# Optimization experiments

Measured on AMD Instinct MI355X. Metric: run time of the kernel, lower is better.

The kernel has to match this reference:

```python
import jax, jax.numpy as jnp
import numpy as np

N = 500_000
B = 8192
D = 128
EPS = 1e-5


def setup_inputs() -> dict:
    key = jax.random.key(0)
    ks = jax.random.split(key, 8)
    h = jax.random.normal(ks[0], (N, D), dtype=jnp.float32)
    batch = jnp.sort(jax.random.randint(ks[1], (N,), 0, B)).astype(jnp.int64)
    vn_h = jax.random.normal(ks[2], (B, D), dtype=jnp.float32)
    # layer 0 MLP params: Linear(D,D) -> LayerNorm(D) -> ReLU -> Linear(D,D)
    W1 = jax.random.normal(ks[3], (D, D), dtype=jnp.float32) * 0.02
    b1 = jnp.zeros((D,), dtype=jnp.float32)
    ln_g = jnp.ones((D,), dtype=jnp.float32)
    ln_b = jnp.zeros((D,), dtype=jnp.float32)
    W2 = jax.random.normal(ks[4], (D, D), dtype=jnp.float32) * 0.02
    b2 = jnp.zeros((D,), dtype=jnp.float32)
    return {"h": h, "batch": batch, "vn_h": vn_h, "W1": W1, "b1": b1,
            "ln_g": ln_g, "ln_b": ln_b, "W2": W2, "b2": b2}


def _layernorm(x, g, b):
    mu = jnp.mean(x, axis=-1, keepdims=True)
    var = jnp.mean(jnp.square(x - mu), axis=-1, keepdims=True)
    return (x - mu) * jax.lax.rsqrt(var + EPS) * g + b


def reference(h, batch, vn_h, W1, b1, ln_g, ln_b, W2, b2):
    batch = batch.astype(jnp.int32)
    # global_mean_pool: segment mean of node features per graph  [B, D]
    seg_sum = jax.ops.segment_sum(h, batch, num_segments=B)
    counts = jax.ops.segment_sum(jnp.ones((h.shape[0],), h.dtype), batch, num_segments=B)
    pooled = seg_sum / jnp.maximum(counts, 1.0)[:, None]
    vn_h_new = pooled + vn_h
    # vn MLP: Linear -> LayerNorm -> ReLU -> Linear
    x = vn_h_new @ W1.T + b1
    x = jax.nn.relu(_layernorm(x, ln_g, ln_b))
    vn_out = x @ W2.T + b2                      # [B, D]
    h_out = h + vn_out[batch]                   # broadcast gather back to nodes
    return h_out, vn_out
```

## Files before the change

### kernel.cpp

```cpp
#include <hip/hip_runtime.h>

#define DIM 128
#define EPS 1e-5f

typedef short           bf16x8 __attribute__((ext_vector_type(8)));
typedef unsigned short  u16x4  __attribute__((ext_vector_type(4)));
typedef float           f32x4  __attribute__((ext_vector_type(4)));

__device__ __forceinline__ unsigned short f2b(float f) {
    unsigned int u = __builtin_bit_cast(unsigned int, f);
    unsigned int r = (u + 0x7FFFu + ((u >> 16) & 1u)) >> 16;
    return (unsigned short)r;
}
__device__ __forceinline__ bf16x8 ldw8(const float* __restrict__ p) {
    f32x4 a = *reinterpret_cast<const f32x4*>(p);
    f32x4 b = *reinterpret_cast<const f32x4*>(p + 4);
    bf16x8 r;
    #pragma unroll
    for (int j = 0; j < 4; ++j) {
        r[j]     = (short)f2b(a[j]);
        r[j + 4] = (short)f2b(b[j]);
    }
    return r;
}

__global__ __launch_bounds__(256) void k_bounds(
    const int* __restrict__ batch, int* __restrict__ bounds, int n_nodes, int nb)
{
    const int idx = blockIdx.x * blockDim.x + threadIdx.x;
    if (idx > n_nodes) return;
    const int cur  = (idx < n_nodes) ? batch[idx] : nb;
    const int prev = (idx > 0) ? batch[idx - 1] : -1;
    for (int b = prev + 1; b <= cur; ++b) bounds[b] = idx;
}

__global__ __launch_bounds__(256) void k_pool(
    const float* __restrict__ h, const int* __restrict__ bounds,
    const float* __restrict__ vn, unsigned short* __restrict__ x_ws, int nb)
{
    const int wid  = (blockIdx.x * blockDim.x + threadIdx.x) >> 6;
    const int lane = threadIdx.x & 63;
    if (wid >= nb) return;
    const int rsub = lane >> 5;
    const int l32  = lane & 31;
    const int s = bounds[wid], e = bounds[wid + 1];

    const f32x4 z4 = (f32x4){0.f, 0.f, 0.f, 0.f};
    f32x4 a0 = z4, a1 = z4, a2 = z4, a3 = z4;
    int n = s;
    for (; n + 7 < e; n += 8) {
        const float* p = h + (size_t)(n + rsub) * DIM + l32 * 4;
        f32x4 x0 = *reinterpret_cast<const f32x4*>(p);
        f32x4 x1 = *reinterpret_cast<const f32x4*>(p + 2 * DIM);
        f32x4 x2 = *reinterpret_cast<const f32x4*>(p + 4 * DIM);
        f32x4 x3 = *reinterpret_cast<const f32x4*>(p + 6 * DIM);
        a0 += x0; a1 += x1; a2 += x2; a3 += x3;
    }
    for (; n + rsub < e; n += 2)
        a0 += *reinterpret_cast<const f32x4*>(h + (size_t)(n + rsub) * DIM + l32 * 4);
    a0 += a1; a2 += a3; a0 += a2;
    #pragma unroll
    for (int c = 0; c < 4; ++c) a0[c] += __shfl_xor(a0[c], 32);

    if (rsub == 0) {
        const int cnt = e - s;
        const float inv = 1.0f / (float)(cnt > 1 ? cnt : 1);
        f32x4 vv = *reinterpret_cast<const f32x4*>(vn + (size_t)wid * DIM + l32 * 4);
        u16x4 ov;
        #pragma unroll
        for (int q = 0; q < 4; ++q) ov[q] = f2b(fmaf(a0[q], inv, vv[q]));
        *reinterpret_cast<u16x4*>(x_ws + (size_t)wid * DIM + l32 * 4) = ov;
    }
}

__global__ __launch_bounds__(256) void k_mlp(
    const unsigned short* __restrict__ x_ws,
    const float* __restrict__ W1, const float* __restrict__ b1,
    const float* __restrict__ lng, const float* __restrict__ lnb,
    const float* __restrict__ W2, const float* __restrict__ b2v,
    float* __restrict__ vn_out)
{
    __shared__ unsigned short zt[4][16][136];

    const int wave  = threadIdx.x >> 6;
    const int lane  = threadIdx.x & 63;
    const int gtile = blockIdx.x * 4 + wave;
    const int row16 = lane & 15;
    const int kgrp  = lane >> 4;

    bf16x8 afrag[4];
    {
        const unsigned short* xp =
            x_ws + (size_t)(gtile * 16 + row16) * DIM + kgrp * 8;
        #pragma unroll
        for (int kk = 0; kk < 4; ++kk)
            afrag[kk] = *reinterpret_cast<const bf16x8*>(xp + kk * 32);
    }
    f32x4 acc[8];
    #pragma unroll
    for (int t = 0; t < 8; ++t) acc[t] = (f32x4){0.f, 0.f, 0.f, 0.f};
    #pragma unroll
    for (int t = 0; t < 8; ++t) {
        const float* wp = W1 + (size_t)(t * 16 + row16) * DIM + kgrp * 8;
        #pragma unroll
        for (int kk = 0; kk < 4; ++kk) {
            bf16x8 bfrag = ldw8(wp + kk * 32);
            acc[t] = __builtin_amdgcn_mfma_f32_16x16x32_bf16(afrag[kk], bfrag, acc[t], 0, 0, 0);
        }
    }

    float b1f[8], gf[8], bf_[8], b2f8[8];
    #pragma unroll
    for (int t = 0; t < 8; ++t) {
        const int f = t * 16 + row16;
        b1f[t]  = b1[f];
        gf[t]   = lng[f];
        bf_[t]  = lnb[f];
        b2f8[t] = b2v[f];
    }
    #pragma unroll
    for (int t = 0; t < 8; ++t)
        #pragma unroll
        for (int r = 0; r < 4; ++r) acc[t][r] += b1f[t];

    #pragma unroll
    for (int r = 0; r < 4; ++r) {
        float sm = 0.f, ss = 0.f;
        #pragma unroll
        for (int t = 0; t < 8; ++t) { sm += acc[t][r]; ss += acc[t][r] * acc[t][r]; }
        #pragma unroll
        for (int m = 1; m <= 8; m <<= 1) {
            sm += __shfl_xor(sm, m);
            ss += __shfl_xor(ss, m);
        }
        const float mu  = sm * (1.0f / 128.0f);
        const float var = ss * (1.0f / 128.0f) - mu * mu;
        const float rs  = rsqrtf(var + EPS);
        const int   gm  = kgrp * 4 + r;
        #pragma unroll
        for (int t = 0; t < 8; ++t) {
            float z = (acc[t][r] - mu) * rs * gf[t] + bf_[t];
            z = fmaxf(z, 0.f);
            zt[wave][gm][t * 16 + row16] = f2b(z);
        }
    }
    __syncthreads();

    bf16x8 afrag2[4];
    #pragma unroll
    for (int kk = 0; kk < 4; ++kk)
        afrag2[kk] = *reinterpret_cast<const bf16x8*>(&zt[wave][row16][kk * 32 + kgrp * 8]);

    f32x4 acc2[8];
    #pragma unroll
    for (int t = 0; t < 8; ++t) acc2[t] = (f32x4){0.f, 0.f, 0.f, 0.f};
    #pragma unroll
    for (int t = 0; t < 8; ++t) {
        const float* wp = W2 + (size_t)(t * 16 + row16) * DIM + kgrp * 8;
        #pragma unroll
        for (int kk = 0; kk < 4; ++kk) {
            bf16x8 bfrag = ldw8(wp + kk * 32);
            acc2[t] = __builtin_amdgcn_mfma_f32_16x16x32_bf16(afrag2[kk], bfrag, acc2[t], 0, 0, 0);
        }
    }

    #pragma unroll
    for (int r = 0; r < 4; ++r) {
        float* op = vn_out + (size_t)(gtile * 16 + kgrp * 4 + r) * DIM + row16;
        #pragma unroll
        for (int t = 0; t < 8; ++t)
            op[t * 16] = acc2[t][r] + b2f8[t];
    }
}

__global__ __launch_bounds__(256) void k_add(
    const float* __restrict__ h, const int* __restrict__ batch,
    const float* __restrict__ vn_out, float* __restrict__ h_out,
    int n_nodes)
{
    const long total = (long)n_nodes * 16;
    for (long u = (long)blockIdx.x * blockDim.x + threadIdx.x; u < total;
         u += (long)gridDim.x * blockDim.x) {
        const int n = (int)(u >> 4);
        const int c = ((int)u & 15) * 8;
        const float* hp = h + (size_t)n * DIM + c;
        f32x4 h0 = *reinterpret_cast<const f32x4*>(hp);
        f32x4 h1 = *reinterpret_cast<const f32x4*>(hp + 4);
        const int b = batch[n];
        const float* vp = vn_out + (size_t)b * DIM + c;
        f32x4 v0 = *reinterpret_cast<const f32x4*>(vp);
        f32x4 v1 = *reinterpret_cast<const f32x4*>(vp + 4);
        float* op = h_out + (size_t)n * DIM + c;
        __builtin_nontemporal_store(h0 + v0, reinterpret_cast<f32x4*>(op));
        __builtin_nontemporal_store(h1 + v1, reinterpret_cast<f32x4*>(op + 4));
    }
}

extern "C" void kernel_launch(void* const* d_in, const int* in_sizes, int n_in,
                              void* d_out, int out_size, void* d_ws, size_t ws_size,
                              hipStream_t stream)
{
    const float* h    = (const float*)d_in[0];
    const int*   bat  = (const int*)d_in[1];
    const float* vn   = (const float*)d_in[2];
    const float* W1   = (const float*)d_in[3];
    const float* b1   = (const float*)d_in[4];
    const float* lng  = (const float*)d_in[5];
    const float* lnb  = (const float*)d_in[6];
    const float* W2   = (const float*)d_in[7];
    const float* b2v  = (const float*)d_in[8];

    const int n_nodes = in_sizes[0] / DIM;
    const int nb      = in_sizes[2] / DIM;

    float* out    = (float*)d_out;
    float* h_out  = out;
    float* vn_out = out + (size_t)n_nodes * DIM;
    int*   bounds = (int*)d_ws;
    unsigned short* x_ws =
        (unsigned short*)((char*)d_ws + ((size_t)(nb + 1) * 4 + 255 & ~255ull));

    k_bounds<<<(n_nodes + 256) / 256, 256, 0, stream>>>(bat, bounds, n_nodes, nb);
    k_pool<<<nb / 4, 256, 0, stream>>>(h, bounds, vn, x_ws, nb);
    k_mlp<<<nb / 64, 256, 0, stream>>>(x_ws, W1, b1, lng, lnb, W2, b2v, vn_out);
    k_add<<<2048, 256, 0, stream>>>(h, bat, vn_out, h_out, n_nodes);
}
```

Before: 160.1 us.

## Fuse pooling, MLP and broadcast-add into one per-graph wave kernel

Replaces the separate pool, MLP and add kernels with a single kernel where each wave owns one graph. The wave sums that graph's nodes, runs both linear layers through MFMA with the pooled row padded into a 16-row tile via lane shuffles, then re-reads the graph's nodes to write h_out. Weights are converted to bf16 once in a small prep kernel instead of on every weight load. This removes the intermediate round trips and the per-node gather of batch indices. In exchange, 15 of the 16 MFMA rows do wasted work, and h is read twice within the same wave, which works best if the second read still hits cache. Writing vn_out and reading it back relies on a vmcnt wait and a volatile load within the wave.

```diff
diff --git a/kernel.cpp b/kernel.cpp
--- a/kernel.cpp
+++ b/kernel.cpp
@@ -3,25 +3,15 @@
 #define DIM 128
 #define EPS 1e-5f
 
-typedef short           bf16x8 __attribute__((ext_vector_type(8)));
-typedef unsigned short  u16x4  __attribute__((ext_vector_type(4)));
-typedef float           f32x4  __attribute__((ext_vector_type(4)));
+typedef short        bf16x8 __attribute__((ext_vector_type(8)));
+typedef unsigned int u32x4  __attribute__((ext_vector_type(4)));
+typedef float        f32x2  __attribute__((ext_vector_type(2)));
+typedef float        f32x4  __attribute__((ext_vector_type(4)));
 
 __device__ __forceinline__ unsigned short f2b(float f) {
     unsigned int u = __builtin_bit_cast(unsigned int, f);
     unsigned int r = (u + 0x7FFFu + ((u >> 16) & 1u)) >> 16;
     return (unsigned short)r;
-}
-__device__ __forceinline__ bf16x8 ldw8(const float* __restrict__ p) {
-    f32x4 a = *reinterpret_cast<const f32x4*>(p);
-    f32x4 b = *reinterpret_cast<const f32x4*>(p + 4);
-    bf16x8 r;
-    #pragma unroll
-    for (int j = 0; j < 4; ++j) {
-        r[j]     = (short)f2b(a[j]);
-        r[j + 4] = (short)f2b(b[j]);
-    }
-    return r;
 }
 
 __global__ __launch_bounds__(256) void k_bounds(
@@ -34,165 +24,172 @@
     for (int b = prev + 1; b <= cur; ++b) bounds[b] = idx;
 }
 
-__global__ __launch_bounds__(256) void k_pool(
+__global__ __launch_bounds__(256) void k_prep(
+    const float* __restrict__ W1, const float* __restrict__ W2,
+    unsigned short* __restrict__ Wb)
+{
+    const int i = blockIdx.x * blockDim.x + threadIdx.x;
+    if (i >= 32768) return;
+    const float v = (i < 16384) ? W1[i] : W2[i - 16384];
+    Wb[i] = f2b(v);
+}
+
+__global__ __launch_bounds__(256, 6) void k_fused(
     const float* __restrict__ h, const int* __restrict__ bounds,
-    const float* __restrict__ vn, unsigned short* __restrict__ x_ws, int nb)
+    const float* __restrict__ vn, const unsigned short* __restrict__ Wb,
+    const float* __restrict__ b1, const float* __restrict__ lng,
+    const float* __restrict__ lnb, const float* __restrict__ b2v,
+    float* __restrict__ vn_out, float* __restrict__ h_out)
 {
     const int wid  = (blockIdx.x * blockDim.x + threadIdx.x) >> 6;
     const int lane = threadIdx.x & 63;
-    if (wid >= nb) return;
-    const int rsub = lane >> 5;
-    const int l32  = lane & 31;
     const int s = bounds[wid], e = bounds[wid + 1];
 
-    const f32x4 z4 = (f32x4){0.f, 0.f, 0.f, 0.f};
-    f32x4 a0 = z4, a1 = z4, a2 = z4, a3 = z4;
+    const f32x2 z2 = (f32x2){0.f, 0.f};
+    f32x2 a0 = z2, a1 = z2, a2 = z2, a3 = z2, a4 = z2, a5 = z2, a6 = z2, a7 = z2;
     int n = s;
-    for (; n + 7 < e; n += 8) {
-        const float* p = h + (size_t)(n + rsub) * DIM + l32 * 4;
-        f32x4 x0 = *reinterpret_cast<const f32x4*>(p);
-        f32x4 x1 = *reinterpret_cast<const f32x4*>(p + 2 * DIM);
-        f32x4 x2 = *reinterpret_cast<const f32x4*>(p + 4 * DIM);
-        f32x4 x3 = *reinterpret_cast<const f32x4*>(p + 6 * DIM);
-        a0 += x0; a1 += x1; a2 += x2; a3 += x3;
-    }
-    for (; n + rsub < e; n += 2)
-        a0 += *reinterpret_cast<const f32x4*>(h + (size_t)(n + rsub) * DIM + l32 * 4);
-    a0 += a1; a2 += a3; a0 += a2;
-    #pragma unroll
-    for (int c = 0; c < 4; ++c) a0[c] += __shfl_xor(a0[c], 32);
-
-    if (rsub == 0) {
-        const int cnt = e - s;
-        const float inv = 1.0f / (float)(cnt > 1 ? cnt : 1);
-        f32x4 vv = *reinterpret_cast<const f32x4*>(vn + (size_t)wid * DIM + l32 * 4);
-        u16x4 ov;
-        #pragma unroll
-        for (int q = 0; q < 4; ++q) ov[q] = f2b(fmaf(a0[q], inv, vv[q]));
-        *reinterpret_cast<u16x4*>(x_ws + (size_t)wid * DIM + l32 * 4) = ov;
-    }
-}
-
-__global__ __launch_bounds__(256) void k_mlp(
-    const unsigned short* __restrict__ x_ws,
-    const float* __restrict__ W1, const float* __restrict__ b1,
-    const float* __restrict__ lng, const float* __restrict__ lnb,
-    const float* __restrict__ W2, const float* __restrict__ b2v,
-    float* __restrict__ vn_out)
-{
-    __shared__ unsigned short zt[4][16][136];
-
-    const int wave  = threadIdx.x >> 6;
-    const int lane  = threadIdx.x & 63;
-    const int gtile = blockIdx.x * 4 + wave;
+    for (; n + 8 <= e; n += 8) {
+        const float* p = h + (size_t)n * DIM + lane * 2;
+        a0 += *reinterpret_cast<const f32x2*>(p);
+        a1 += *reinterpret_cast<const f32x2*>(p + DIM);
+        a2 += *reinterpret_cast<const f32x2*>(p + 2 * DIM);
+        a3 += *reinterpret_cast<const f32x2*>(p + 3 * DIM);
+        a4 += *reinterpret_cast<const f32x2*>(p + 4 * DIM);
+        a5 += *reinterpret_cast<const f32x2*>(p + 5 * DIM);
+        a6 += *reinterpret_cast<const f32x2*>(p + 6 * DIM);
+        a7 += *reinterpret_cast<const f32x2*>(p + 7 * DIM);
+    }
+    for (; n < e; ++n)
+        a0 += *reinterpret_cast<const f32x2*>(h + (size_t)n * DIM + lane * 2);
+    a0 += a1; a2 += a3; a4 += a5; a6 += a7; a0 += a2; a4 += a6; a0 += a4;
+
+    const int cnt = e - s;
+    const float inv = 1.0f / (float)(cnt > 1 ? cnt : 1);
+    f32x2 vv = *reinterpret_cast<const f32x2*>(vn + (size_t)wid * DIM + lane * 2);
+    const unsigned int x01 =
+        (unsigned int)f2b(fmaf(a0[0], inv, vv[0])) |
+        ((unsigned int)f2b(fmaf(a0[1], inv, vv[1])) << 16);
+
     const int row16 = lane & 15;
     const int kgrp  = lane >> 4;
 
-    bf16x8 afrag[4];
-    {
-        const unsigned short* xp =
-            x_ws + (size_t)(gtile * 16 + row16) * DIM + kgrp * 8;
-        #pragma unroll
-        for (int kk = 0; kk < 4; ++kk)
-            afrag[kk] = *reinterpret_cast<const bf16x8*>(xp + kk * 32);
-    }
-    f32x4 acc[8];
-    #pragma unroll
-    for (int t = 0; t < 8; ++t) acc[t] = (f32x4){0.f, 0.f, 0.f, 0.f};
+    bf16x8 af[4];
+    #pragma unroll
+    for (int kt = 0; kt < 4; ++kt) {
+        const int sbase = kt * 16 + kgrp * 4;
+        u32x4 w;
+        w[0] = __shfl(x01, sbase + 0);
+        w[1] = __shfl(x01, sbase + 1);
+        w[2] = __shfl(x01, sbase + 2);
+        w[3] = __shfl(x01, sbase + 3);
+        af[kt] = __builtin_bit_cast(bf16x8, w);
+    }
+
+    f32x4 C[8];
+    #pragma unroll
+    for (int t = 0; t < 8; ++t) C[t] = (f32x4){0.f, 0.f, 0.f, 0.f};
     #pragma unroll
     for (int t = 0; t < 8; ++t) {
-        const float* wp = W1 + (size_t)(t * 16 + row16) * DIM + kgrp * 8;
-        #pragma unroll
-        for (int kk = 0; kk < 4; ++kk) {
-            bf16x8 bfrag = ldw8(wp + kk * 32);
-            acc[t] = __builtin_amdgcn_mfma_f32_16x16x32_bf16(afrag[kk], bfrag, acc[t], 0, 0, 0);
+        const unsigned short* wr = Wb + (size_t)(t * 16 + row16) * DIM + kgrp * 8;
+        #pragma unroll
+        for (int kt = 0; kt < 4; ++kt) {
+            bf16x8 bf = *reinterpret_cast<const bf16x8*>(wr + kt * 32);
+            C[t] = __builtin_amdgcn_mfma_f32_16x16x32_bf16(af[kt], bf, C[t], 0, 0, 0);
         }
     }
 
-    float b1f[8], gf[8], bf_[8], b2f8[8];
+    float y[8];
+    float gf[8], bf_[8], b2f8[8];
     #pragma unroll
     for (int t = 0; t < 8; ++t) {
         const int f = t * 16 + row16;
-        b1f[t]  = b1[f];
+        y[t]    = C[t][0] + b1[f];
         gf[t]   = lng[f];
         bf_[t]  = lnb[f];
         b2f8[t] = b2v[f];
     }
-    #pragma unroll
-    for (int t = 0; t < 8; ++t)
-        #pragma unroll
-        for (int r = 0; r < 4; ++r) acc[t][r] += b1f[t];
-
-    #pragma unroll
-    for (int r = 0; r < 4; ++r) {
-        float sm = 0.f, ss = 0.f;
-        #pragma unroll
-        for (int t = 0; t < 8; ++t) { sm += acc[t][r]; ss += acc[t][r] * acc[t][r]; }
-        #pragma unroll
-        for (int m = 1; m <= 8; m <<= 1) {
-            sm += __shfl_xor(sm, m);
-            ss += __shfl_xor(ss, m);
+
+    float sm = 0.f, ss = 0.f;
+    #pragma unroll
+    for (int t = 0; t < 8; ++t) { sm += y[t]; ss += y[t] * y[t]; }
+    #pragma unroll
+    for (int m = 1; m <= 8; m <<= 1) {
+        sm += __shfl_xor(sm, m);
+        ss += __shfl_xor(ss, m);
+    }
+    const float mu  = sm * (1.0f / 128.0f);
+    const float var = ss * (1.0f / 128.0f) - mu * mu;
+    const float rs  = rsqrtf(var + EPS);
+
+    unsigned int zp[4];
+    #pragma unroll
+    for (int kt = 0; kt < 4; ++kt) {
+        float zl = fmaxf((y[2 * kt]     - mu) * rs * gf[2 * kt]     + bf_[2 * kt],     0.f);
+        float zh = fmaxf((y[2 * kt + 1] - mu) * rs * gf[2 * kt + 1] + bf_[2 * kt + 1], 0.f);
+        zp[kt] = (unsigned int)f2b(zl) | ((unsigned int)f2b(zh) << 16);
+    }
+
+    const unsigned int hsel = kgrp >> 1;
+    const int sbase2 = (kgrp & 1) * 8;
+    bf16x8 zf[4];
+    #pragma unroll
+    for (int kt = 0; kt < 4; ++kt) {
+        u32x4 w;
+        #pragma unroll
+        for (int c2 = 0; c2 < 4; ++c2) {
+            unsigned int q0 = __shfl(zp[kt], sbase2 + 2 * c2);
+            unsigned int q1 = __shfl(zp[kt], sbase2 + 2 * c2 + 1);
+            unsigned int e0 = hsel ? (q0 >> 16) : (q0 & 0xFFFFu);
+            unsigned int e1 = hsel ? (q1 >> 16) : (q1 & 0xFFFFu);
+            w[c2] = e0 | (e1 << 16);
         }
-        const float mu  = sm * (1.0f / 128.0f);
-        const float var = ss * (1.0f / 128.0f) - mu * mu;
-        const float rs  = rsqrtf(var + EPS);
-        const int   gm  = kgrp * 4 + r;
-        #pragma unroll
-        for (int t = 0; t < 8; ++t) {
-            float z = (acc[t][r] - mu) * rs * gf[t] + bf_[t];
-            z = fmaxf(z, 0.f);
-            zt[wave][gm][t * 16 + row16] = f2b(z);
+        zf[kt] = __builtin_bit_cast(bf16x8, w);
+    }
+
+    f32x4 C2[8];
+    #pragma unroll
+    for (int t = 0; t < 8; ++t) C2[t] = (f32x4){0.f, 0.f, 0.f, 0.f};
+    #pragma unroll
+    for (int t = 0; t < 8; ++t) {
+        const unsigned short* wr =
+            Wb + 16384 + (size_t)(t * 16 + row16) * DIM + kgrp * 8;
+        #pragma unroll
+        for (int kt = 0; kt < 4; ++kt) {
+            bf16x8 bf = *reinterpret_cast<const bf16x8*>(wr + kt * 32);
+            C2[t] = __builtin_amdgcn_mfma_f32_16x16x32_bf16(zf[kt], bf, C2[t], 0, 0, 0);
         }
     }
-    __syncthreads();
-
-    bf16x8 afrag2[4];
-    #pragma unroll
-    for (int kk = 0; kk < 4; ++kk)
-        afrag2[kk] = *reinterpret_cast<const bf16x8*>(&zt[wave][row16][kk * 32 + kgrp * 8]);
-
-    f32x4 acc2[8];
-    #pragma unroll
-    for (int t = 0; t < 8; ++t) acc2[t] = (f32x4){0.f, 0.f, 0.f, 0.f};
-    #pragma unroll
-    for (int t = 0; t < 8; ++t) {
-        const float* wp = W2 + (size_t)(t * 16 + row16) * DIM + kgrp * 8;
-        #pragma unroll
-        for (int kk = 0; kk < 4; ++kk) {
-            bf16x8 bfrag = ldw8(wp + kk * 32);
-            acc2[t] = __builtin_amdgcn_mfma_f32_16x16x32_bf16(afrag2[kk], bfrag, acc2[t], 0, 0, 0);
-        }
-    }
-
-    #pragma unroll
-    for (int r = 0; r < 4; ++r) {
-        float* op = vn_out + (size_t)(gtile * 16 + kgrp * 4 + r) * DIM + row16;
+
+    if (lane < 16) {
         #pragma unroll
         for (int t = 0; t < 8; ++t)
-            op[t * 16] = acc2[t][r] + b2f8[t];
-    }
-}
-
-__global__ __launch_bounds__(256) void k_add(
-    const float* __restrict__ h, const int* __restrict__ batch,
-    const float* __restrict__ vn_out, float* __restrict__ h_out,
-    int n_nodes)
-{
-    const long total = (long)n_nodes * 16;
-    for (long u = (long)blockIdx.x * blockDim.x + threadIdx.x; u < total;
-         u += (long)gridDim.x * blockDim.x) {
-        const int n = (int)(u >> 4);
-        const int c = ((int)u & 15) * 8;
-        const float* hp = h + (size_t)n * DIM + c;
-        f32x4 h0 = *reinterpret_cast<const f32x4*>(hp);
-        f32x4 h1 = *reinterpret_cast<const f32x4*>(hp + 4);
-        const int b = batch[n];
-        const float* vp = vn_out + (size_t)b * DIM + c;
-        f32x4 v0 = *reinterpret_cast<const f32x4*>(vp);
-        f32x4 v1 = *reinterpret_cast<const f32x4*>(vp + 4);
-        float* op = h_out + (size_t)n * DIM + c;
-        __builtin_nontemporal_store(h0 + v0, reinterpret_cast<f32x4*>(op));
-        __builtin_nontemporal_store(h1 + v1, reinterpret_cast<f32x4*>(op + 4));
+            vn_out[(size_t)wid * DIM + t * 16 + row16] = C2[t][0] + b2f8[t];
+    }
+
+    asm volatile("s_waitcnt vmcnt(0)" ::: "memory");
+    volatile const float* vo = vn_out + (size_t)wid * DIM + lane * 2;
+    const float w0 = vo[0];
+    const float w1 = vo[1];
+    const f32x2 w = (f32x2){w0, w1};
+
+    n = s;
+    for (; n + 4 <= e; n += 4) {
+        const float* p = h + (size_t)n * DIM + lane * 2;
+        f32x2 r0 = *reinterpret_cast<const f32x2*>(p);
+        f32x2 r1 = *reinterpret_cast<const f32x2*>(p + DIM);
+        f32x2 r2 = *reinterpret_cast<const f32x2*>(p + 2 * DIM);
+        f32x2 r3 = *reinterpret_cast<const f32x2*>(p + 3 * DIM);
+        float* q = h_out + (size_t)n * DIM + lane * 2;
+        __builtin_nontemporal_store(r0 + w, reinterpret_cast<f32x2*>(q));
+        __builtin_nontemporal_store(r1 + w, reinterpret_cast<f32x2*>(q + DIM));
+        __builtin_nontemporal_store(r2 + w, reinterpret_cast<f32x2*>(q + 2 * DIM));
+        __builtin_nontemporal_store(r3 + w, reinterpret_cast<f32x2*>(q + 3 * DIM));
+    }
+    for (; n < e; ++n) {
+        const float* p = h + (size_t)n * DIM + lane * 2;
+        f32x2 r0 = *reinterpret_cast<const f32x2*>(p);
+        float* q = h_out + (size_t)n * DIM + lane * 2;
+        __builtin_nontemporal_store(r0 + w, reinterpret_cast<f32x2*>(q));
     }
 }
 
@@ -216,12 +213,13 @@
     float* out    = (float*)d_out;
     float* h_out  = out;
     float* vn_out = out + (size_t)n_nodes * DIM;
-    int*   bounds = (int*)d_ws;
-    unsigned short* x_ws =
-        (unsigned short*)((char*)d_ws + ((size_t)(nb + 1) * 4 + 255 & ~255ull));
+
+    int* bounds = (int*)d_ws;
+    unsigned short* Wb = (unsigned short*)
+        ((char*)d_ws + (((size_t)(nb + 1) * 4 + 255) & ~(size_t)255));
 
     k_bounds<<<(n_nodes + 256) / 256, 256, 0, stream>>>(bat, bounds, n_nodes, nb);
-    k_pool<<<nb / 4, 256, 0, stream>>>(h, bounds, vn, x_ws, nb);
-    k_mlp<<<nb / 64, 256, 0, stream>>>(x_ws, W1, b1, lng, lnb, W2, b2v, vn_out);
-    k_add<<<2048, 256, 0, stream>>>(h, bat, vn_out, h_out, n_nodes);
-}
+    k_prep<<<128, 256, 0, stream>>>(W1, W2, Wb);
+    k_fused<<<nb * 64 / 256, 256, 0, stream>>>(h, bounds, vn, Wb,
+                                               b1, lng, lnb, b2v, vn_out, h_out);
+}
```

After: 180.5 us. +12.8%, slower.

## Replace per-graph pooling with row-linear LDS-atomic segment sum and reverse add loop

Applied to the files above, without the earlier changes.

Segment pooling now walks node rows in fixed chunks of 256 per block. It accumulates into shared-memory bins with LDS atomics and flushes them to a global fp32 accumulator placed in the start of the h_out buffer. The mean and vn addition are folded into the MLP's A-fragment load, using the bounds array for counts. The goal is to balance work across blocks regardless of segment sizes. The broadcast-add kernel now iterates in reverse so that the last-written h rows, likely still in cache, are reused first. The cost is an extra zero kernel, many global atomics at block boundaries, and reliance on the accumulator region being fully overwritten by k_add.

```diff
diff --git a/kernel.cpp b/kernel.cpp
--- a/kernel.cpp
+++ b/kernel.cpp
@@ -2,10 +2,11 @@
 
 #define DIM 128
 #define EPS 1e-5f
-
-typedef short           bf16x8 __attribute__((ext_vector_type(8)));
-typedef unsigned short  u16x4  __attribute__((ext_vector_type(4)));
-typedef float           f32x4  __attribute__((ext_vector_type(4)));
+#define RPB 256
+
+typedef short  bf16x8 __attribute__((ext_vector_type(8)));
+typedef float  f32x2  __attribute__((ext_vector_type(2)));
+typedef float  f32x4  __attribute__((ext_vector_type(4)));
 
 __device__ __forceinline__ unsigned short f2b(float f) {
     unsigned int u = __builtin_bit_cast(unsigned int, f);
@@ -22,6 +23,12 @@
         r[j + 4] = (short)f2b(b[j]);
     }
     return r;
+}
+
+__global__ __launch_bounds__(256) void k_zero(float* __restrict__ accum)
+{
+    const int i = blockIdx.x * blockDim.x + threadIdx.x;
+    *reinterpret_cast<f32x4*>(accum + (size_t)i * 4) = (f32x4){0.f, 0.f, 0.f, 0.f};
 }
 
 __global__ __launch_bounds__(256) void k_bounds(
@@ -34,47 +41,56 @@
     for (int b = prev + 1; b <= cur; ++b) bounds[b] = idx;
 }
 
-__global__ __launch_bounds__(256) void k_pool(
-    const float* __restrict__ h, const int* __restrict__ bounds,
-    const float* __restrict__ vn, unsigned short* __restrict__ x_ws, int nb)
-{
-    const int wid  = (blockIdx.x * blockDim.x + threadIdx.x) >> 6;
-    const int lane = threadIdx.x & 63;
-    if (wid >= nb) return;
-    const int rsub = lane >> 5;
-    const int l32  = lane & 31;
-    const int s = bounds[wid], e = bounds[wid + 1];
-
-    const f32x4 z4 = (f32x4){0.f, 0.f, 0.f, 0.f};
-    f32x4 a0 = z4, a1 = z4, a2 = z4, a3 = z4;
-    int n = s;
-    for (; n + 7 < e; n += 8) {
-        const float* p = h + (size_t)(n + rsub) * DIM + l32 * 4;
-        f32x4 x0 = *reinterpret_cast<const f32x4*>(p);
-        f32x4 x1 = *reinterpret_cast<const f32x4*>(p + 2 * DIM);
-        f32x4 x2 = *reinterpret_cast<const f32x4*>(p + 4 * DIM);
-        f32x4 x3 = *reinterpret_cast<const f32x4*>(p + 6 * DIM);
-        a0 += x0; a1 += x1; a2 += x2; a3 += x3;
-    }
-    for (; n + rsub < e; n += 2)
-        a0 += *reinterpret_cast<const f32x4*>(h + (size_t)(n + rsub) * DIM + l32 * 4);
-    a0 += a1; a2 += a3; a0 += a2;
-    #pragma unroll
-    for (int c = 0; c < 4; ++c) a0[c] += __shfl_xor(a0[c], 32);
-
-    if (rsub == 0) {
-        const int cnt = e - s;
-        const float inv = 1.0f / (float)(cnt > 1 ? cnt : 1);
-        f32x4 vv = *reinterpret_cast<const f32x4*>(vn + (size_t)wid * DIM + l32 * 4);
-        u16x4 ov;
-        #pragma unroll
-        for (int q = 0; q < 4; ++q) ov[q] = f2b(fmaf(a0[q], inv, vv[q]));
-        *reinterpret_cast<u16x4*>(x_ws + (size_t)wid * DIM + l32 * 4) = ov;
+__global__ __launch_bounds__(256) void k_pool_lin(
+    const float* __restrict__ h, const int* __restrict__ batch,
+    float* __restrict__ accum, int n_nodes)
+{
+    __shared__ float acc[32][DIM];
+    __shared__ int   sbat[RPB];
+
+    const int tid = threadIdx.x;
+    const int r0  = blockIdx.x * RPB;
+
+    float* af = &acc[0][0];
+    #pragma unroll
+    for (int i = 0; i < 16; ++i) af[tid + 256 * i] = 0.f;
+
+    const int rend = min(RPB, n_nodes - r0);
+    if (tid < rend) sbat[tid] = batch[r0 + tid];
+    __syncthreads();
+
+    const int g0   = sbat[0];
+    const int wave = tid >> 6, lane = tid & 63;
+    const int lr_beg = wave * 64;
+    const int lr_end = min(lr_beg + 64, rend);
+
+    #pragma unroll 4
+    for (int lr = lr_beg; lr < lr_end; ++lr) {
+        f32x2 v = *reinterpret_cast<const f32x2*>(
+            h + (size_t)(r0 + lr) * DIM + lane * 2);
+        const int gl = sbat[lr] - g0;
+        if (gl < 32) {
+            atomicAdd(&acc[gl][lane * 2],     v[0]);
+            atomicAdd(&acc[gl][lane * 2 + 1], v[1]);
+        } else {
+            atomicAdd(&accum[(size_t)(g0 + gl) * DIM + lane * 2],     v[0]);
+            atomicAdd(&accum[(size_t)(g0 + gl) * DIM + lane * 2 + 1], v[1]);
+        }
+    }
+    __syncthreads();
+
+    int gspan = sbat[rend - 1] - g0 + 1;
+    if (gspan > 32) gspan = 32;
+    for (int idx = tid; idx < (gspan << 7); idx += 256) {
+        const int gl = idx >> 7, c = idx & 127;
+        const float v = acc[gl][c];
+        if (v != 0.f) atomicAdd(&accum[(size_t)(g0 + gl) * DIM + c], v);
     }
 }
 
 __global__ __launch_bounds__(256) void k_mlp(
-    const unsigned short* __restrict__ x_ws,
+    const float* __restrict__ accum, const int* __restrict__ bounds,
+    const float* __restrict__ vn,
     const float* __restrict__ W1, const float* __restrict__ b1,
     const float* __restrict__ lng, const float* __restrict__ lnb,
     const float* __restrict__ W2, const float* __restrict__ b2v,
@@ -88,14 +104,26 @@
     const int row16 = lane & 15;
     const int kgrp  = lane >> 4;
 
+    const int g   = gtile * 16 + row16;
+    const int cnt = bounds[g + 1] - bounds[g];
+    const float inv = 1.0f / (float)(cnt > 1 ? cnt : 1);
+
     bf16x8 afrag[4];
-    {
-        const unsigned short* xp =
-            x_ws + (size_t)(gtile * 16 + row16) * DIM + kgrp * 8;
-        #pragma unroll
-        for (int kk = 0; kk < 4; ++kk)
-            afrag[kk] = *reinterpret_cast<const bf16x8*>(xp + kk * 32);
-    }
+    #pragma unroll
+    for (int kk = 0; kk < 4; ++kk) {
+        const float* ap = accum + (size_t)g * DIM + kgrp * 8 + kk * 32;
+        const float* vp = vn    + (size_t)g * DIM + kgrp * 8 + kk * 32;
+        f32x4 s0 = *reinterpret_cast<const f32x4*>(ap);
+        f32x4 s1 = *reinterpret_cast<const f32x4*>(ap + 4);
+        f32x4 u0 = *reinterpret_cast<const f32x4*>(vp);
+        f32x4 u1 = *reinterpret_cast<const f32x4*>(vp + 4);
+        #pragma unroll
+        for (int j = 0; j < 4; ++j) {
+            afrag[kk][j]     = (short)f2b(fmaf(s0[j], inv, u0[j]));
+            afrag[kk][j + 4] = (short)f2b(fmaf(s1[j], inv, u1[j]));
+        }
+    }
+
     f32x4 acc[8];
     #pragma unroll
     for (int t = 0; t < 8; ++t) acc[t] = (f32x4){0.f, 0.f, 0.f, 0.f};
@@ -179,8 +207,11 @@
     int n_nodes)
 {
     const long total = (long)n_nodes * 16;
-    for (long u = (long)blockIdx.x * blockDim.x + threadIdx.x; u < total;
-         u += (long)gridDim.x * blockDim.x) {
+    const long GS    = (long)gridDim.x * blockDim.x;
+    const long gtid  = (long)blockIdx.x * blockDim.x + threadIdx.x;
+    for (long base = ((total + GS - 1) / GS - 1) * GS; base >= 0; base -= GS) {
+        const long u = base + gtid;
+        if (u >= total) continue;
         const int n = (int)(u >> 4);
         const int c = ((int)u & 15) * 8;
         const float* hp = h + (size_t)n * DIM + c;
@@ -216,12 +247,13 @@
     float* out    = (float*)d_out;
     float* h_out  = out;
     float* vn_out = out + (size_t)n_nodes * DIM;
+    float* accum  = out;
     int*   bounds = (int*)d_ws;
-    unsigned short* x_ws =
-        (unsigned short*)((char*)d_ws + ((size_t)(nb + 1) * 4 + 255 & ~255ull));
-
+
+    k_zero<<<(nb * DIM) / 1024, 256, 0, stream>>>(accum);
     k_bounds<<<(n_nodes + 256) / 256, 256, 0, stream>>>(bat, bounds, n_nodes, nb);
-    k_pool<<<nb / 4, 256, 0, stream>>>(h, bounds, vn, x_ws, nb);
-    k_mlp<<<nb / 64, 256, 0, stream>>>(x_ws, W1, b1, lng, lnb, W2, b2v, vn_out);
+    k_pool_lin<<<(n_nodes + RPB - 1) / RPB, 256, 0, stream>>>(h, bat, accum, n_nodes);
+    k_mlp<<<nb / 64, 256, 0, stream>>>(accum, bounds, vn, W1, b1, lng, lnb,
+                                       W2, b2v, vn_out);
     k_add<<<2048, 256, 0, stream>>>(h, bat, vn_out, h_out, n_nodes);
 }
```

Result: slower. 463.1 us (+189.4%).
